# Performance work log

Measured on AMD Instinct MI355X. Metric: run time of the kernel, lower is better.

Reference implementation:

```python
import jax, jax.numpy as jnp
import numpy as np

LEVEL = 10
S = 2 ** (LEVEL + 1)   # face side (ring size)
HS = S // 2            # half side (rows per face)
B = 2
F = 5                  # five faces of the icosahedral rhombus layout


def setup_inputs() -> dict:
    key = jax.random.key(0)
    ks = jax.random.split(key, 10)
    mk = lambda k, shp: jax.random.normal(k, shp, dtype=jnp.float32)
    return {
        "x": mk(ks[0], (B, F, HS, S)),
        "poles": mk(ks[1], (B, 2, 1)),
        "w_inner": mk(ks[2], (6, HS - 2, S - 2)),
        "w_east": mk(ks[3], (6, HS - 1)),
        "w_cn": mk(ks[4], (6,)),
        "w_ne": mk(ks[5], (6, HS - 2)),
        "w_nne": mk(ks[6], (6,)),
        "w_nw": mk(ks[7], (6, HS - 2)),
        "w_nww": mk(ks[8], (6,)),
        "w_west": mk(ks[9], (6, HS - 1)),
    }


def _wp(face_slice, xi, w):
    # wrap-previous face diff: out[f] = (in[f-1 mod 5] - x[f]) * w
    return (jnp.roll(face_slice, 1, axis=1) - xi) * w


def _wn(face_slice, xi, w):
    # wrap-next face diff: out[f] = (in[f+1 mod 5] - x[f]) * w
    return (jnp.roll(face_slice, -1, axis=1) - xi) * w


def reference(x, poles, w_inner, w_east, w_cn, w_ne, w_nne, w_nw, w_nww, w_west):
    Bb, Ff, hs, s = x.shape
    out = jnp.zeros((Bb, 4, Ff, hs, s), x.dtype)

    # ---- interior patch (all neighbors in-face) ----
    xi = x[:, :, 1:-1, 1:-1]                                  # [B,5,HS-2,S-2]
    d0 = (x[:, :, :-2, :-2] - xi) * w_inner[0]
    d1 = (x[:, :, 2:, 2:] - xi) * w_inner[1]
    d2 = (x[:, :, :-2, 1:-1] - xi) * w_inner[2] + (x[:, :, 1:-1, 2:] - xi) * w_inner[3]
    d3 = (x[:, :, 1:-1, :-2] - xi) * w_inner[4] + (x[:, :, 2:, 1:-1] - xi) * w_inner[5]
    out = out.at[:, :, :, 1:-1, 1:-1].set(jnp.stack([d0, d1, d2, d3], axis=1))

    # ---- east seam: row 0, cols 1:HS ----
    xi = x[:, :, 0, 1:hs]                                     # [B,5,HS-1]
    d0 = _wp(x[:, :, hs - 1, hs:s - 1], xi, w_east[0])
    d1 = (x[:, :, 1, 2:hs + 1] - xi) * w_east[1]
    d2 = _wp(x[:, :, hs - 1, hs + 1:s], xi, w_east[2]) + (x[:, :, 0, 2:hs + 1] - xi) * w_east[3]
    d3 = (x[:, :, 0, 0:hs - 1] - xi) * w_east[4] + (x[:, :, 1, 1:hs] - xi) * w_east[5]
    out = out.at[:, :, :, 0, 1:hs].set(jnp.stack([d0, d1, d2, d3], axis=1))

    # ---- corner-north vertex: row 0, col HS ----
    xi = x[:, :, 0, hs]                                       # [B,5]
    d0 = _wp(x[:, :, hs - 1, s - 1], xi, w_cn[0])
    d1 = (x[:, :, 1, hs + 1] - xi) * w_cn[1]
    d2 = (x[:, :, 0, hs + 1] - xi) * w_cn[2]
    d3 = (x[:, :, 0, hs - 1] - xi) * w_cn[3] + (x[:, :, 1, hs] - xi) * w_cn[4]
    out = out.at[:, :, :, 0, hs].set(jnp.stack([d0, d1, d2, d3], axis=1))

    # ---- north-east seam: row 0, cols HS+1:S-1 ----
    xi = x[:, :, 0, hs + 1:s - 1]                             # [B,5,HS-2]
    d0 = _wp(x[:, :, hs - 2:0:-1, s - 1], xi, w_ne[0]) + _wp(x[:, :, hs - 1:1:-1, s - 1], xi, w_ne[1])
    d1 = (x[:, :, 1, hs + 2:s] - xi) * w_ne[2] + (x[:, :, 1, hs + 1:s - 1] - xi) * w_ne[3]
    d2 = (x[:, :, 0, hs + 2:s] - xi) * w_ne[4]
    d3 = (x[:, :, 0, hs:s - 2] - xi) * w_ne[5]
    out = out.at[:, :, :, 0, hs + 1:s - 1].set(jnp.stack([d0, d1, d2, d3], axis=1))

    # ---- north-north-east corner (touches pole): row 0, col S-1 ----
    xi = x[:, :, 0, s - 1]                                    # [B,5]
    d0 = _wp(x[:, :, 0, s - 1], xi, w_nne[0]) + _wp(x[:, :, 1, s - 1], xi, w_nne[1])
    d1 = _wn(x[:, :, 0, s - 1], xi, w_nne[2]) + (x[:, :, 1, s - 1] - xi) * w_nne[3]
    d2 = (poles[:, 1] - xi) * w_nne[4]
    d3 = (x[:, :, 0, s - 2] - xi) * w_nne[5]
    out = out.at[:, :, :, 0, s - 1].set(jnp.stack([d0, d1, d2, d3], axis=1))

    # ---- north-west seam: rows 1:HS-1, col S-1 ----
    xi = x[:, :, 1:hs - 1, s - 1]                             # [B,5,HS-2]
    d0 = (x[:, :, 0:hs - 2, s - 2] - xi) * w_nw[0]
    d1 = _wn(x[:, :, 0, s - 2:hs:-1], xi, w_nw[1])
    d2 = (x[:, :, 0:hs - 2, s - 1] - xi) * w_nw[2] + _wn(x[:, :, 0, s - 1:hs + 1:-1], xi, w_nw[3])
    d3 = (x[:, :, 1:hs - 1, s - 2] - xi) * w_nw[4] + (x[:, :, 2:hs, s - 1] - xi) * w_nw[5]
    out = out.at[:, :, :, 1:hs - 1, s - 1].set(jnp.stack([d0, d1, d2, d3], axis=1))

    # ---- north-west-west corner: row HS-1, col S-1 ----
    xi = x[:, :, hs - 1, s - 1]                               # [B,5]
    d0 = (x[:, :, hs - 2, s - 2] - xi) * w_nww[0]
    d1 = _wn(x[:, :, 0, hs], xi, w_nww[1])
    d2 = (x[:, :, hs - 2, s - 1] - xi) * w_nww[2] + _wn(x[:, :, 0, hs + 1], xi, w_nww[3])
    d3 = (x[:, :, hs - 1, s - 2] - xi) * w_nww[4] + _wn(x[:, :, 0, hs - 1], xi, w_nww[5])
    out = out.at[:, :, :, hs - 1, s - 1].set(jnp.stack([d0, d1, d2, d3], axis=1))

    # ---- west seam: row HS-1, cols HS:S-1 ----
    xi = x[:, :, hs - 1, hs:s - 1]                            # [B,5,HS-1]
    d0 = (x[:, :, hs - 2, hs - 1:s - 2] - xi) * w_west[0]
    d1 = _wn(x[:, :, 0, 1:hs], xi, w_west[1])
    d2 = (x[:, :, hs - 2, hs:s - 1] - xi) * w_west[2] + (x[:, :, hs - 1, hs + 1:s] - xi) * w_west[3]
    d3 = (x[:, :, hs - 1, hs - 1:s - 2] - xi) * w_west[4] + _wn(x[:, :, 0, 0:hs - 1], xi, w_west[5])
    out = out.at[:, :, :, hs - 1, hs:s - 1].set(jnp.stack([d0, d1, d2, d3], axis=1))

    return out
```

## Files before the change

### kernel.cpp

```cpp
#include <hip/hip_runtime.h>

constexpr int S  = 2048;
constexpr int HS = 1024;
constexpr int B  = 2;
constexpr int F  = 5;
constexpr int PL = HS * S;
constexpr int OD = F * PL;
constexpr int WI = (HS - 2) * (S - 2);


__global__ __launch_bounds__(256)
void icok(const float* __restrict__ x, const float* __restrict__ poles,
          const float* __restrict__ w_inner, const float* __restrict__ w_east,
          const float* __restrict__ w_cn, const float* __restrict__ w_ne,
          const float* __restrict__ w_nne, const float* __restrict__ w_nw,
          const float* __restrict__ w_nww, const float* __restrict__ w_west,
          float* __restrict__ out)
{
    const int gid = blockIdx.x * 256 + threadIdx.x;
    const int i = gid >> 11;
    const int j = gid & (S - 1);

    if (j == 0 || (i == HS - 1 && j < HS)) {
        for (int b = 0; b < B; ++b) {
#pragma unroll
            for (int f = 0; f < F; ++f) {
                float* ob = out + b * (4 * OD) + f * PL + i * S + j;
                ob[0] = 0.f; ob[OD] = 0.f; ob[2 * OD] = 0.f; ob[3 * OD] = 0.f;
            }
        }
        return;
    }

    if (i > 0 && i < HS - 1 && j < S - 1) {
        const int wo = (i - 1) * (S - 2) + (j - 1);
        const float w0 = w_inner[wo];
        const float w1 = w_inner[wo + WI];
        const float w2 = w_inner[wo + 2 * WI];
        const float w3 = w_inner[wo + 3 * WI];
        const float w4 = w_inner[wo + 4 * WI];
        const float w5 = w_inner[wo + 5 * WI];
        const int rm = (i - 1) * S + j;
        const int rc = i * S + j;
        const int rp = (i + 1) * S + j;
        for (int b = 0; b < B; ++b) {
#pragma unroll
            for (int f = 0; f < F; ++f) {
                const float* xb = x + (b * F + f) * PL;
                const float xi = xb[rc];
                const float d0 = (xb[rm - 1] - xi) * w0;
                const float d1 = (xb[rp + 1] - xi) * w1;
                const float d2 = (xb[rm] - xi) * w2 + (xb[rc + 1] - xi) * w3;
                const float d3 = (xb[rc - 1] - xi) * w4 + (xb[rp] - xi) * w5;
                float* ob = out + b * (4 * OD) + f * PL + rc;
                ob[0] = d0; ob[OD] = d1; ob[2 * OD] = d2; ob[3 * OD] = d3;
            }
        }
        return;
    }

    if (i == 0) {
        if (j < HS) {
            const int t = j - 1;
            const float w0 = w_east[t];
            const float w1 = w_east[t + (HS - 1)];
            const float w2 = w_east[t + 2 * (HS - 1)];
            const float w3 = w_east[t + 3 * (HS - 1)];
            const float w4 = w_east[t + 4 * (HS - 1)];
            const float w5 = w_east[t + 5 * (HS - 1)];
            for (int b = 0; b < B; ++b) {
#pragma unroll
                for (int f = 0; f < F; ++f) {
                    const int fm = (f == 0) ? F - 1 : f - 1;
                    const float* xb  = x + (b * F + f) * PL;
                    const float* xmb = x + (b * F + fm) * PL;
                    const float xi = xb[j];
                    const float d0 = (xmb[(HS - 1) * S + HS + t] - xi) * w0;
                    const float d1 = (xb[S + 2 + t] - xi) * w1;
                    const float d2 = (xmb[(HS - 1) * S + HS + 1 + t] - xi) * w2
                                   + (xb[2 + t] - xi) * w3;
                    const float d3 = (xb[t] - xi) * w4 + (xb[S + 1 + t] - xi) * w5;
                    float* ob = out + b * (4 * OD) + f * PL + j;
                    ob[0] = d0; ob[OD] = d1; ob[2 * OD] = d2; ob[3 * OD] = d3;
                }
            }
        } else if (j == HS) {
            const float w0 = w_cn[0], w1 = w_cn[1], w2 = w_cn[2], w3 = w_cn[3], w4 = w_cn[4];
            for (int b = 0; b < B; ++b) {
#pragma unroll
                for (int f = 0; f < F; ++f) {
                    const int fm = (f == 0) ? F - 1 : f - 1;
                    const float* xb  = x + (b * F + f) * PL;
                    const float* xmb = x + (b * F + fm) * PL;
                    const float xi = xb[HS];
                    const float d0 = (xmb[(HS - 1) * S + S - 1] - xi) * w0;
                    const float d1 = (xb[S + HS + 1] - xi) * w1;
                    const float d2 = (xb[HS + 1] - xi) * w2;
                    const float d3 = (xb[HS - 1] - xi) * w3 + (xb[S + HS] - xi) * w4;
                    float* ob = out + b * (4 * OD) + f * PL + HS;
                    ob[0] = d0; ob[OD] = d1; ob[2 * OD] = d2; ob[3 * OD] = d3;
                }
            }
        } else if (j < S - 1) {
            const int t = j - HS - 1;
            const float w0 = w_ne[t];
            const float w1 = w_ne[t + (HS - 2)];
            const float w2 = w_ne[t + 2 * (HS - 2)];
            const float w3 = w_ne[t + 3 * (HS - 2)];
            const float w4 = w_ne[t + 4 * (HS - 2)];
            const float w5 = w_ne[t + 5 * (HS - 2)];
            for (int b = 0; b < B; ++b) {
#pragma unroll
                for (int f = 0; f < F; ++f) {
                    const int fm = (f == 0) ? F - 1 : f - 1;
                    const float* xb  = x + (b * F + f) * PL;
                    const float* xmb = x + (b * F + fm) * PL;
                    const float xi = xb[j];
                    const float d0 = (xmb[(HS - 2 - t) * S + S - 1] - xi) * w0
                                   + (xmb[(HS - 1 - t) * S + S - 1] - xi) * w1;
                    const float d1 = (xb[S + HS + 2 + t] - xi) * w2
                                   + (xb[S + HS + 1 + t] - xi) * w3;
                    const float d2 = (xb[HS + 2 + t] - xi) * w4;
                    const float d3 = (xb[HS + t] - xi) * w5;
                    float* ob = out + b * (4 * OD) + f * PL + j;
                    ob[0] = d0; ob[OD] = d1; ob[2 * OD] = d2; ob[3 * OD] = d3;
                }
            }
        } else {
            const float w0 = w_nne[0], w1 = w_nne[1], w2 = w_nne[2],
                        w3 = w_nne[3], w4 = w_nne[4], w5 = w_nne[5];
            for (int b = 0; b < B; ++b) {
#pragma unroll
                for (int f = 0; f < F; ++f) {
                    const int fm = (f == 0) ? F - 1 : f - 1;
                    const int fp = (f == F - 1) ? 0 : f + 1;
                    const float* xb  = x + (b * F + f) * PL;
                    const float* xmb = x + (b * F + fm) * PL;
                    const float* xpb = x + (b * F + fp) * PL;
                    const float xi = xb[S - 1];
                    const float d0 = (xmb[S - 1] - xi) * w0 + (xmb[S + S - 1] - xi) * w1;
                    const float d1 = (xpb[S - 1] - xi) * w2 + (xb[S + S - 1] - xi) * w3;
                    const float d2 = (poles[b * 2 + 1] - xi) * w4;
                    const float d3 = (xb[S - 2] - xi) * w5;
                    float* ob = out + b * (4 * OD) + f * PL + (S - 1);
                    ob[0] = d0; ob[OD] = d1; ob[2 * OD] = d2; ob[3 * OD] = d3;
                }
            }
        }
        return;
    }

    if (i == HS - 1) {
        if (j < S - 1) {
            const int t = j - HS;
            const float w0 = w_west[t];
            const float w1 = w_west[t + (HS - 1)];
            const float w2 = w_west[t + 2 * (HS - 1)];
            const float w3 = w_west[t + 3 * (HS - 1)];
            const float w4 = w_west[t + 4 * (HS - 1)];
            const float w5 = w_west[t + 5 * (HS - 1)];
            for (int b = 0; b < B; ++b) {
#pragma unroll
                for (int f = 0; f < F; ++f) {
                    const int fp = (f == F - 1) ? 0 : f + 1;
                    const float* xb  = x + (b * F + f) * PL;
                    const float* xpb = x + (b * F + fp) * PL;
                    const float xi = xb[(HS - 1) * S + j];
                    const float d0 = (xb[(HS - 2) * S + HS - 1 + t] - xi) * w0;
                    const float d1 = (xpb[1 + t] - xi) * w1;
                    const float d2 = (xb[(HS - 2) * S + HS + t] - xi) * w2
                                   + (xb[(HS - 1) * S + HS + 1 + t] - xi) * w3;
                    const float d3 = (xb[(HS - 1) * S + HS - 1 + t] - xi) * w4
                                   + (xpb[t] - xi) * w5;
                    float* ob = out + b * (4 * OD) + f * PL + (HS - 1) * S + j;
                    ob[0] = d0; ob[OD] = d1; ob[2 * OD] = d2; ob[3 * OD] = d3;
                }
            }
        } else {
            const float w0 = w_nww[0], w1 = w_nww[1], w2 = w_nww[2],
                        w3 = w_nww[3], w4 = w_nww[4], w5 = w_nww[5];
            for (int b = 0; b < B; ++b) {
#pragma unroll
                for (int f = 0; f < F; ++f) {
                    const int fp = (f == F - 1) ? 0 : f + 1;
                    const float* xb  = x + (b * F + f) * PL;
                    const float* xpb = x + (b * F + fp) * PL;
                    const float xi = xb[(HS - 1) * S + S - 1];
                    const float d0 = (xb[(HS - 2) * S + S - 2] - xi) * w0;
                    const float d1 = (xpb[HS] - xi) * w1;
                    const float d2 = (xb[(HS - 2) * S + S - 1] - xi) * w2
                                   + (xpb[HS + 1] - xi) * w3;
                    const float d3 = (xb[(HS - 1) * S + S - 2] - xi) * w4
                                   + (xpb[HS - 1] - xi) * w5;
                    float* ob = out + b * (4 * OD) + f * PL + (HS - 1) * S + (S - 1);
                    ob[0] = d0; ob[OD] = d1; ob[2 * OD] = d2; ob[3 * OD] = d3;
                }
            }
        }
        return;
    }

    {
        const int t = i - 1;
        const float w0 = w_nw[t];
        const float w1 = w_nw[t + (HS - 2)];
        const float w2 = w_nw[t + 2 * (HS - 2)];
        const float w3 = w_nw[t + 3 * (HS - 2)];
        const float w4 = w_nw[t + 4 * (HS - 2)];
        const float w5 = w_nw[t + 5 * (HS - 2)];
        for (int b = 0; b < B; ++b) {
#pragma unroll
            for (int f = 0; f < F; ++f) {
                const int fp = (f == F - 1) ? 0 : f + 1;
                const float* xb  = x + (b * F + f) * PL;
                const float* xpb = x + (b * F + fp) * PL;
                const float xi = xb[i * S + S - 1];
                const float d0 = (xb[(i - 1) * S + S - 2] - xi) * w0;
                const float d1 = (xpb[S - 2 - t] - xi) * w1;
                const float d2 = (xb[(i - 1) * S + S - 1] - xi) * w2
                               + (xpb[S - 1 - t] - xi) * w3;
                const float d3 = (xb[i * S + S - 2] - xi) * w4
                               + (xb[(i + 1) * S + S - 1] - xi) * w5;
                float* ob = out + b * (4 * OD) + f * PL + i * S + (S - 1);
                ob[0] = d0; ob[OD] = d1; ob[2 * OD] = d2; ob[3 * OD] = d3;
            }
        }
    }
}

extern "C" void kernel_launch(void* const* d_in, const int* in_sizes, int n_in,
                              void* d_out, int out_size, void* d_ws, size_t ws_size,
                              hipStream_t stream) {
    const float* x       = (const float*)d_in[0];
    const float* poles   = (const float*)d_in[1];
    const float* w_inner = (const float*)d_in[2];
    const float* w_east  = (const float*)d_in[3];
    const float* w_cn    = (const float*)d_in[4];
    const float* w_ne    = (const float*)d_in[5];
    const float* w_nne   = (const float*)d_in[6];
    const float* w_nw    = (const float*)d_in[7];
    const float* w_nww   = (const float*)d_in[8];
    const float* w_west  = (const float*)d_in[9];
    float* out = (float*)d_out;

    const int total = HS * S;
    dim3 grid(total / 256), block(256);
    hipLaunchKernelGGL(icok, grid, block, 0, stream,
                       x, poles, w_inner, w_east, w_cn, w_ne, w_nne, w_nw,
                       w_nww, w_west, out);
}
```

Baseline: 459.7 us.

## Vectorize interior stencil with float4 loads and nontemporal stores, separate boundary path

Interior points are now processed four columns per thread using 128-bit loads of x and w_inner and nontemporal vector stores, with shifted neighbours built from register shuffles plus scalar edge loads. Block indices are swizzled across rows, and boundary rows and columns go to a small set of extra blocks that call the original scalar routine. The aim is fewer memory instructions, full-width coalesced traffic, and less cache pollution from the large output write. The cost is extra index logic and unaligned w_inner vector loads, since that array has row stride S-2.

```diff
diff --git a/kernel.cpp b/kernel.cpp
--- a/kernel.cpp
+++ b/kernel.cpp
@@ -8,19 +8,22 @@
 constexpr int OD = F * PL;
 constexpr int WI = (HS - 2) * (S - 2);
 
-
-__global__ __launch_bounds__(256)
-void icok(const float* __restrict__ x, const float* __restrict__ poles,
-          const float* __restrict__ w_inner, const float* __restrict__ w_east,
-          const float* __restrict__ w_cn, const float* __restrict__ w_ne,
-          const float* __restrict__ w_nne, const float* __restrict__ w_nw,
-          const float* __restrict__ w_nww, const float* __restrict__ w_west,
-          float* __restrict__ out)
+typedef float v4  __attribute__((ext_vector_type(4)));
+typedef float v4u __attribute__((ext_vector_type(4), aligned(4)));
+
+__device__ __forceinline__ void st_nt(float* p, v4 v) {
+    __builtin_nontemporal_store(v, (v4*)p);
+}
+
+__device__ void scalar_point(
+    int i, int j,
+    const float* __restrict__ x, const float* __restrict__ poles,
+    const float* __restrict__ w_inner, const float* __restrict__ w_east,
+    const float* __restrict__ w_cn, const float* __restrict__ w_ne,
+    const float* __restrict__ w_nne, const float* __restrict__ w_nw,
+    const float* __restrict__ w_nww, const float* __restrict__ w_west,
+    float* __restrict__ out)
 {
-    const int gid = blockIdx.x * 256 + threadIdx.x;
-    const int i = gid >> 11;
-    const int j = gid & (S - 1);
-
     if (j == 0 || (i == HS - 1 && j < HS)) {
         for (int b = 0; b < B; ++b) {
 #pragma unroll
@@ -226,6 +229,81 @@
             }
         }
     }
+}
+
+__global__ __launch_bounds__(256)
+void icok(const float* __restrict__ x, const float* __restrict__ poles,
+          const float* __restrict__ w_inner, const float* __restrict__ w_east,
+          const float* __restrict__ w_cn, const float* __restrict__ w_ne,
+          const float* __restrict__ w_nne, const float* __restrict__ w_nw,
+          const float* __restrict__ w_nww, const float* __restrict__ w_west,
+          float* __restrict__ out)
+{
+    const int p = blockIdx.x;
+
+    if (p < 2048) {
+        const int l = ((p & 7) << 8) | (p >> 3);
+        const int i = 1 + (l >> 1);
+        if (i > HS - 2) return;
+        const int jt = ((l & 1) << 8) | threadIdx.x;
+        if (jt == 0 || jt == 511) return;
+        const int j0 = jt << 2;
+
+        const int wo = (i - 1) * (S - 2) + (j0 - 1);
+        const v4 w0v = *(const v4u*)(w_inner + wo);
+        const v4 w1v = *(const v4u*)(w_inner + wo + WI);
+        const v4 w2v = *(const v4u*)(w_inner + wo + 2 * WI);
+        const v4 w3v = *(const v4u*)(w_inner + wo + 3 * WI);
+        const v4 w4v = *(const v4u*)(w_inner + wo + 4 * WI);
+        const v4 w5v = *(const v4u*)(w_inner + wo + 5 * WI);
+
+        const int rm = (i - 1) * S + j0;
+        const int rc = i * S + j0;
+        const int rp = (i + 1) * S + j0;
+
+        for (int b = 0; b < B; ++b) {
+#pragma unroll
+            for (int f = 0; f < F; ++f) {
+                const float* xb = x + (b * F + f) * PL;
+                const v4 c = *(const v4*)(xb + rc);
+                const v4 m = *(const v4*)(xb + rm);
+                const v4 pv = *(const v4*)(xb + rp);
+                const float ml = xb[rm - 1];
+                const float cl = xb[rc - 1];
+                const float cr = xb[rc + 4];
+                const float pr = xb[rp + 4];
+                const v4 xmm1 = {ml, m.x, m.y, m.z};
+                const v4 xpp1 = {pv.y, pv.z, pv.w, pr};
+                const v4 xcm1 = {cl, c.x, c.y, c.z};
+                const v4 xcp1 = {c.y, c.z, c.w, cr};
+
+                const v4 d0 = (xmm1 - c) * w0v;
+                const v4 d1 = (xpp1 - c) * w1v;
+                const v4 d2 = (m - c) * w2v + (xcp1 - c) * w3v;
+                const v4 d3 = (xcm1 - c) * w4v + (pv - c) * w5v;
+
+                float* ob = out + b * (4 * OD) + f * PL + rc;
+                st_nt(ob, d0);
+                st_nt(ob + OD, d1);
+                st_nt(ob + 2 * OD, d2);
+                st_nt(ob + 3 * OD, d3);
+            }
+        }
+        return;
+    }
+
+    const int e = (p - 2048) * 256 + threadIdx.x;
+    int i, j;
+    if (e < 2048)      { i = 0;      j = e; }
+    else if (e < 4096) { i = HS - 1; j = e - 2048; }
+    else if (e < 4096 + 8 * (HS - 2)) {
+        const int t = e - 4096;
+        i = 1 + (t >> 3);
+        const int c = t & 7;
+        j = (c < 4) ? c : (2040 + c);
+    } else return;
+    scalar_point(i, j, x, poles, w_inner, w_east, w_cn, w_ne, w_nne,
+                 w_nw, w_nww, w_west, out);
 }
 
 extern "C" void kernel_launch(void* const* d_in, const int* in_sizes, int n_in,
@@ -243,8 +321,7 @@
     const float* w_west  = (const float*)d_in[9];
     float* out = (float*)d_out;
 
-    const int total = HS * S;
-    dim3 grid(total / 256), block(256);
+    dim3 grid(2048 + 48), block(256);
     hipLaunchKernelGGL(icok, grid, block, 0, stream,
                        x, poles, w_inner, w_east, w_cn, w_ne, w_nne, w_nw,
                        w_nww, w_west, out);
```

Measured after the change: 458.2 us. Within noise of the previous version (-0.3%).
